# Kernel tuning notes

Hardware: AMD Instinct MI355X
Metric: run time of the kernel (lower is better)

The kernel has to match this reference:

```python
import jax, jax.numpy as jnp
import numpy as np

EPS = 1e-5

def _ln(x, g=None, b=None):
    m = x.mean(-1, keepdims=True)
    v = x.var(-1, keepdims=True)
    y = (x - m) / jnp.sqrt(v + EPS)
    if g is not None:
        y = y * g + b
    return y

def setup_inputs() -> dict:
    B, N, D, E, NC = 32, 256, 1024, 4096, 16
    key = jax.random.key(0)
    ks = iter(jax.random.split(key, 24))
    def rn(shape, s=0.02):
        return jax.random.normal(next(ks), shape, jnp.float32) * s
    return dict(
        h=jax.random.normal(next(ks), (B, N, D), jnp.float32),
        Wpp=rn((D, E)), bpp=jnp.zeros(E), Wsp=rn((D, E)), bsp=jnp.zeros(E),
        Wq=rn((E, E)), bq=jnp.zeros(E),
        Wk=rn((E, E)), bk=jnp.zeros(E),
        Wv=rn((E, E)), bv=jnp.zeros(E),
        g_pfs=jnp.ones(D + E), b_pfs=jnp.zeros(D + E),
        Wpfs=rn((D + E, D)), bpfs=jnp.zeros(D),
        g_sfs=jnp.ones(E), b_sfs=jnp.zeros(E),
        Wsfs=rn((E, D)), bsfs=jnp.zeros(D),
        Wpc=rn((D, NC)), bpc=jnp.zeros(NC),
        Wc0=rn((NC, 8, D)), bc0=jnp.zeros((NC, 8)),
        Wc1=rn((NC, 16, D)), bc1=jnp.zeros((NC, 16)),
        Wc2=rn((NC, 32, D)), bc2=jnp.zeros((NC, 32)),
    )

def reference(h, Wpp, bpp, Wsp, bsp, Wq, bq, Wk, bk, Wv, bv,
              g_pfs, b_pfs, Wpfs, bpfs, g_sfs, b_sfs, Wsfs, bsfs,
              Wpc, bpc, Wc0, bc0, Wc1, bc1, Wc2, bc2):
    B, N, D = h.shape
    H = 4
    E = Wpp.shape[1]
    hd = E // H
    scale = hd ** -0.5
    gelu = lambda x: jax.nn.gelu(x, approximate=False)  # torch exact GELU
    pp = gelu(h @ Wpp + bpp)                  # [B,N,E]
    sp = gelu(h @ Wsp + bsp)                  # [B,N,E]
    Q = (pp @ Wq + bq).reshape(B, N, H, hd)
    K = (sp @ Wk + bk).reshape(B, N, H, hd)
    V = (sp @ Wv + bv).reshape(B, N, H, hd)
    attn = jax.nn.softmax(jnp.einsum('bqhd,bkhd->bhqk', Q, K) * scale, axis=-1)
    intf = jnp.einsum('bhqk,bkhd->bqhd', attn, V).reshape(B, N, E)
    intf = _ln(intf)                          # F.layer_norm, no affine
    pvec = _ln((_ln(jnp.concatenate([h, intf], -1), g_pfs, b_pfs) @ Wpfs + bpfs).mean(1))  # [B,D]
    svec = _ln((_ln(sp, g_sfs, b_sfs) @ Wsfs + bsfs).mean(1))                               # [B,D]
    parent_logits = pvec @ Wpc + bpc          # [B,NC]
    y_hat = jnp.argmax(parent_logits, axis=1) # argmax(softmax) == argmax(logits)
    # routed child heads: gather per-sample weight by parent argmax, batched matvec
    child = tuple(
        jnp.einsum('bd,bnd->bn', svec, W[y_hat]) + b[y_hat]
        for W, b in ((Wc0, bc0), (Wc1, bc1), (Wc2, bc2))
    )
    return (parent_logits,) + child + (pvec, svec)
```

## Files before the change

kernel.cpp:

```cpp
#include <hip/hip_runtime.h>
#include <hip/hip_bf16.h>

typedef __bf16 bf16x8 __attribute__((ext_vector_type(8)));
typedef float f32x4 __attribute__((ext_vector_type(4)));
typedef unsigned long long u64;

#define EPSV 1e-5f

__device__ __forceinline__ float bf2f(unsigned short u){
  unsigned int x = ((unsigned int)u) << 16;
  return __builtin_bit_cast(float, x);
}
__device__ __forceinline__ unsigned short f2bf(float f){
  __bf16 b = (__bf16)f;
  return __builtin_bit_cast(unsigned short, b);
}
__device__ __forceinline__ float gelu_exact(float x){
  return 0.5f * x * (1.0f + erff(x * 0.7071067811865476f));
}
__device__ __forceinline__ void gload_lds16(const void* g, void* l){
  __builtin_amdgcn_global_load_lds((const __attribute__((address_space(1))) unsigned int*)g,
                                   (__attribute__((address_space(3))) unsigned int*)l, 16, 0, 0);
}

#define LGKM0() do{ asm volatile("s_waitcnt lgkmcnt(0)" ::: "memory"); __builtin_amdgcn_sched_barrier(0); }while(0)

template<int MODE>
__global__ __launch_bounds__(512, 2)
void gemm256(const unsigned short* __restrict__ A, const unsigned short* __restrict__ B,
             const float* __restrict__ bias, void* __restrict__ Cv,
             int Kd, int lda, int ldb, int ldc)
{
  __shared__ char smem[131072];
  const int t = threadIdx.x;
  const int w = t >> 6, l = t & 63;
  const int wm = w >> 2, wn = w & 3;
  const int lr = l & 15, lg = l >> 4;
  const int nbx = gridDim.x;
  const int nwg = nbx * gridDim.y;
  int bid = blockIdx.y*nbx + blockIdx.x;
  if ((nwg & 7) == 0) bid = (bid & 7)*(nwg >> 3) + (bid >> 3);
  const int bm0 = (bid / nbx) * 256, bn0 = (bid % nbx) * 256;
  const int nk = Kd >> 6;

  const int srow = t >> 3;
  const int sslot = t & 7;

  f32x4 acc[8][4];
  #pragma unroll
  for (int i=0;i<8;++i){
    #pragma unroll
    for (int j=0;j<4;++j){ f32x4 zz = {0.f,0.f,0.f,0.f}; acc[i][j] = zz; }
  }
  bf16x8 a0[4][2], a1[4][2], b0[2][2], b1[2][2];

  auto stage = [&](int kt, int mat, int hf, int q){
    if (kt >= nk) return;
    const int r_h = q*64 + srow;
    const int s_ = sslot ^ ((r_h >> 1) & 7);
    const unsigned short* gp = (mat ? B + (size_t)(bn0 + hf*128 + r_h)*ldb
                                    : A + (size_t)(bm0 + hf*128 + r_h)*lda)
                               + (kt << 6) + s_*8;
    char* lp = smem + mat*65536 + (kt&1)*32768 + hf*16384 + q*8192 + t*16;
    gload_lds16((const void*)gp, (void*)lp);
  };
  auto rdA = [&](int d, int fm, int kk)->bf16x8{
    const int r = fm*16 + lr;
    const int s_ = (kk*4 + lg) ^ ((r >> 1) & 7);
    return *(const bf16x8*)(smem + d*32768 + wm*16384 + r*128 + s_*16);
  };
  auto rdB = [&](int d, int fn, int kk)->bf16x8{
    const int r = (wn&1)*64 + fn*16 + lr;
    const int s_ = (kk*4 + lg) ^ ((r >> 1) & 7);
    return *(const bf16x8*)(smem + 65536 + d*32768 + (wn>>1)*16384 + r*128 + s_*16);
  };

  auto ktile = [&](int kt, int d){
    #pragma unroll
    for (int fm=0; fm<4; ++fm){ a0[fm][0] = rdA(d, fm, 0); a0[fm][1] = rdA(d, fm, 1); }
    #pragma unroll
    for (int fn=0; fn<2; ++fn){ b0[fn][0] = rdB(d, fn, 0); b0[fn][1] = rdB(d, fn, 1); }
    stage(kt+1, 0, 0, 1); stage(kt+1, 0, 1, 1);
    __builtin_amdgcn_s_barrier();
    LGKM0();
    __builtin_amdgcn_s_setprio(1);
    #pragma unroll
    for (int fm=0; fm<4; ++fm)
      #pragma unroll
      for (int fn=0; fn<2; ++fn)
        #pragma unroll
        for (int kk=0; kk<2; ++kk)
          acc[fm][fn] = __builtin_amdgcn_mfma_f32_16x16x32_bf16(a0[fm][kk], b0[fn][kk], acc[fm][fn], 0,0,0);
    __builtin_amdgcn_s_setprio(0);
    __builtin_amdgcn_s_barrier();
    #pragma unroll
    for (int fn=0; fn<2; ++fn){ b1[fn][0] = rdB(d, fn+2, 0); b1[fn][1] = rdB(d, fn+2, 1); }
    stage(kt+2, 0, 0, 0); stage(kt+2, 0, 1, 0);
    __builtin_amdgcn_s_barrier();
    LGKM0();
    __builtin_amdgcn_s_setprio(1);
    #pragma unroll
    for (int fm=0; fm<4; ++fm)
      #pragma unroll
      for (int fn=0; fn<2; ++fn)
        #pragma unroll
        for (int kk=0; kk<2; ++kk)
          acc[fm][fn+2] = __builtin_amdgcn_mfma_f32_16x16x32_bf16(a0[fm][kk], b1[fn][kk], acc[fm][fn+2], 0,0,0);
    __builtin_amdgcn_s_setprio(0);
    __builtin_amdgcn_s_barrier();
    #pragma unroll
    for (int fm=0; fm<4; ++fm){ a1[fm][0] = rdA(d, fm+4, 0); a1[fm][1] = rdA(d, fm+4, 1); }
    stage(kt+2, 1, 0, 0); stage(kt+2, 1, 1, 0);
    __builtin_amdgcn_s_barrier();
    LGKM0();
    __builtin_amdgcn_s_setprio(1);
    #pragma unroll
    for (int fm=0; fm<4; ++fm)
      #pragma unroll
      for (int fn=0; fn<2; ++fn)
        #pragma unroll
        for (int kk=0; kk<2; ++kk)
          acc[fm+4][fn+2] = __builtin_amdgcn_mfma_f32_16x16x32_bf16(a1[fm][kk], b1[fn][kk], acc[fm+4][fn+2], 0,0,0);
    __builtin_amdgcn_s_setprio(0);
    __builtin_amdgcn_s_barrier();
    stage(kt+2, 1, 0, 1); stage(kt+2, 1, 1, 1);
    __builtin_amdgcn_s_setprio(1);
    #pragma unroll
    for (int fm=0; fm<4; ++fm)
      #pragma unroll
      for (int fn=0; fn<2; ++fn)
        #pragma unroll
        for (int kk=0; kk<2; ++kk)
          acc[fm+4][fn] = __builtin_amdgcn_mfma_f32_16x16x32_bf16(a1[fm][kk], b0[fn][kk], acc[fm+4][fn], 0,0,0);
    __builtin_amdgcn_s_setprio(0);
    if (kt + 2 < nk) { asm volatile("s_waitcnt vmcnt(6)" ::: "memory"); }
    else             { asm volatile("s_waitcnt vmcnt(0)" ::: "memory"); }
    __builtin_amdgcn_s_barrier();
  };

  stage(0,0,0,0); stage(0,0,1,0); stage(0,0,0,1); stage(0,0,1,1);
  stage(0,1,0,0); stage(0,1,1,0); stage(0,1,0,1); stage(0,1,1,1);
  stage(1,0,0,0); stage(1,0,1,0);
  stage(1,1,0,0); stage(1,1,1,0); stage(1,1,0,1); stage(1,1,1,1);
  asm volatile("s_waitcnt vmcnt(6)" ::: "memory");
  __builtin_amdgcn_s_barrier();

  for (int kt = 0; kt < nk; kt += 2){ ktile(kt, 0); ktile(kt+1, 1); }

  #pragma unroll
  for (int fm=0; fm<8; ++fm){
    #pragma unroll
    for (int fn=0; fn<4; ++fn){
      const int row0 = bm0 + wm*128 + fm*16 + lg*4;
      const int col  = bn0 + wn*64 + fn*16 + lr;
      f32x4 v = acc[fm][fn];
      if constexpr (MODE == 3){
        unsigned short* C = (unsigned short*)Cv;
        const float bb = bias[col];
        u64 pack = 0;
        #pragma unroll
        for (int j=0;j<4;++j) pack |= (u64)f2bf(v[j] + bb) << (16*j);
        *(u64*)(C + (size_t)col*256 + (size_t)(row0>>8)*1048576 + (row0&255)) = pack;
      } else {
        unsigned short* C = (unsigned short*)Cv;
        const float bb = bias[col];
        #pragma unroll
        for (int j=0;j<4;++j){
          float x = v[j] + bb;
          if constexpr (MODE==0) x = gelu_exact(x);
          C[(size_t)(row0+j)*ldc + col] = f2bf(x);
        }
      }
    }
  }
}

template<int MODE>
__global__ __launch_bounds__(256)
void gemm_bt(const unsigned short* __restrict__ A, const unsigned short* __restrict__ B,
             const float* __restrict__ bias, void* __restrict__ Cv,
             int Kd, int lda, int ldb, int ldc,
             long sA2, long sA1, long sB2, long sB1, long sC2, long sC1,
             float scale)
{
  __shared__ unsigned short lds[2][2][4096];
  const int t = threadIdx.x;
  const int w = t >> 6, l = t & 63;
  const int z = blockIdx.z;
  A += (size_t)(z>>2)*sA2 + (size_t)(z&3)*sA1;
  B += (size_t)(z>>2)*sB2 + (size_t)(z&3)*sB1;
  const int bm0 = blockIdx.y * 128, bn0 = blockIdx.x * 128;
  const int nk = Kd >> 5;

  const int sr = l >> 2;
  const int ss = l & 3;

  f32x4 acc[4][4];
  #pragma unroll
  for (int i=0;i<4;++i){
    #pragma unroll
    for (int j=0;j<4;++j){ f32x4 zz = {0.f,0.f,0.f,0.f}; acc[i][j] = zz; }
  }

  const int wm = w >> 1, wn = w & 1;
  const int lr = l & 15, lg = l >> 4;

  auto stage = [&](int kt, int bb){
    const int k0 = kt << 5;
    #pragma unroll
    for (int i=0;i<2;++i){
      const int r  = w*32 + i*16 + sr;
      const int sa = ss ^ ((r>>1)&3);
      const unsigned short* ga = A + (size_t)(bm0 + r)*lda + (k0 + sa*8);
      gload_lds16((const void*)ga, (void*)((char*)&lds[bb][0][0] + w*2048 + i*1024));
      const unsigned short* gb = B + (size_t)(bn0 + r)*ldb + (k0 + sa*8);
      gload_lds16((const void*)gb, (void*)((char*)&lds[bb][1][0] + w*2048 + i*1024));
    }
  };

  int buf = 0;
  stage(0, 0);
  for (int kt=0; kt<nk; ++kt){
    __syncthreads();
    if (kt+1 < nk) stage(kt+1, buf^1);
    bf16x8 av[4], bv[4];
    #pragma unroll
    for (int fm=0; fm<4; ++fm){
      const int row = wm*64 + fm*16 + lr;
      const int sl  = lg ^ ((row>>1)&3);
      av[fm] = *(const bf16x8*)((const char*)&lds[buf][0][0] + row*64 + sl*16);
    }
    #pragma unroll
    for (int fn=0; fn<4; ++fn){
      const int col = wn*64 + fn*16 + lr;
      const int sl  = lg ^ ((col>>1)&3);
      bv[fn] = *(const bf16x8*)((const char*)&lds[buf][1][0] + col*64 + sl*16);
    }
    #pragma unroll
    for (int fm=0; fm<4; ++fm){
      #pragma unroll
      for (int fn=0; fn<4; ++fn)
        acc[fm][fn] = __builtin_amdgcn_mfma_f32_16x16x32_bf16(av[fm], bv[fn], acc[fm][fn], 0,0,0);
    }
    buf ^= 1;
  }

  const size_t coff = (size_t)(z>>2)*sC2 + (size_t)(z&3)*sC1;
  #pragma unroll
  for (int fm=0; fm<4; ++fm){
    #pragma unroll
    for (int fn=0; fn<4; ++fn){
      const int row0 = bm0 + wm*64 + fm*16 + lg*4;
      const int col  = bn0 + wn*64 + fn*16 + lr;
      f32x4 v = acc[fm][fn];
      if constexpr (MODE == 2){
        float* C = (float*)Cv + coff;
        #pragma unroll
        for (int j=0;j<4;++j) C[(size_t)(row0+j)*ldc + col] = v[j]*scale;
      }
    }
  }
}

__global__ __launch_bounds__(256)
void k_convh(const float* __restrict__ in, unsigned short* __restrict__ out){
  const size_t id = (size_t)blockIdx.x*256 + threadIdx.x;
  float4 v = ((const float4*)in)[id];
  u64 pack = (u64)f2bf(v.x) | ((u64)f2bf(v.y)<<16) | ((u64)f2bf(v.z)<<32) | ((u64)f2bf(v.w)<<48);
  *(u64*)(out + id*4) = pack;
}

__global__ __launch_bounds__(256)
void k_tconv(const float* __restrict__ W, unsigned short* __restrict__ Wt, int Kd, int N){
  __shared__ float lt[64][65];
  const int t = threadIdx.x;
  const int n0 = blockIdx.x*64, k0 = blockIdx.y*64;
  #pragma unroll
  for (int i=0;i<16;++i){
    int lin = i*256 + t; int r = lin>>6, c = lin&63;
    lt[r][c] = W[(size_t)(k0+r)*N + n0 + c];
  }
  __syncthreads();
  #pragma unroll
  for (int i=0;i<16;++i){
    int lin = i*256 + t; int n = lin>>6, k = lin&63;
    Wt[(size_t)(n0+n)*Kd + k0 + k] = f2bf(lt[k][n]);
  }
}

__global__ __launch_bounds__(256)
void k_softmax(const float* __restrict__ S, unsigned short* __restrict__ P){
  const int t = threadIdx.x, w = t>>6, l = t&63;
  const size_t row = (size_t)blockIdx.x*4 + w;
  float4 v = *(const float4*)(S + row*256 + l*4);
  float m = fmaxf(fmaxf(v.x,v.y), fmaxf(v.z,v.w));
  #pragma unroll
  for (int off=32; off; off>>=1) m = fmaxf(m, __shfl_xor(m, off));
  float e0 = expf(v.x-m), e1 = expf(v.y-m), e2 = expf(v.z-m), e3 = expf(v.w-m);
  float s = e0+e1+e2+e3;
  #pragma unroll
  for (int off=32; off; off>>=1) s += __shfl_xor(s, off);
  const float inv = 1.0f/s;
  u64 pack = (u64)f2bf(e0*inv) | ((u64)f2bf(e1*inv)<<16) | ((u64)f2bf(e2*inv)<<32) | ((u64)f2bf(e3*inv)<<48);
  *(u64*)(P + row*256 + l*4) = pack;
}

__device__ __forceinline__ void blkred2(float& a, float& b, float* sred, int t){
  #pragma unroll
  for (int off=32; off; off>>=1){ a += __shfl_xor(a, off); b += __shfl_xor(b, off); }
  __syncthreads();
  if ((t&63)==0){ sred[(t>>6)*2] = a; sred[(t>>6)*2+1] = b; }
  __syncthreads();
  a = sred[0]+sred[2]+sred[4]+sred[6];
  b = sred[1]+sred[3]+sred[5]+sred[7];
}

__global__ __launch_bounds__(256)
void k_stats(const float* __restrict__ h, const float* __restrict__ intf,
             const unsigned short* __restrict__ sp,
             const float* __restrict__ g_pfs, const float* __restrict__ b_pfs,
             const float* __restrict__ g_sfs, const float* __restrict__ b_sfs,
             float* __restrict__ part_p, float* __restrict__ part_s, int g0)
{
  __shared__ float sred[8];
  const int bl = blockIdx.x, grp = blockIdx.y, t = threadIdx.x;
  float zacc[20], wacc[16];
  #pragma unroll
  for (int j=0;j<20;++j) zacc[j]=0.f;
  #pragma unroll
  for (int j=0;j<16;++j) wacc[j]=0.f;
  for (int rr=0; rr<32; ++rr){
    const size_t r = (size_t)bl*256 + grp*32 + rr;
    float hv[4], iv[16], sv[16];
    #pragma unroll
    for (int j=0;j<4;++j) hv[j] = h[r*1024 + j*256 + t];
    float s1=0.f, s2=0.f;
    #pragma unroll
    for (int j=0;j<16;++j){ float x = intf[r*4096 + j*256 + t]; iv[j]=x; s1+=x; s2+=x*x; }
    blkred2(s1,s2,sred,t);
    const float m1 = s1*(1.f/4096.f);
    const float rs1 = rsqrtf(fmaxf(s2*(1.f/4096.f) - m1*m1, 0.f) + EPSV);
    float t1=0.f, t2=0.f;
    #pragma unroll
    for (int j=0;j<4;++j){ t1 += hv[j]; t2 += hv[j]*hv[j]; }
    #pragma unroll
    for (int j=0;j<16;++j){ float y = (iv[j]-m1)*rs1; iv[j]=y; t1+=y; t2+=y*y; }
    blkred2(t1,t2,sred,t);
    const float m2 = t1*(1.f/5120.f);
    const float rs2 = rsqrtf(fmaxf(t2*(1.f/5120.f) - m2*m2, 0.f) + EPSV);
    #pragma unroll
    for (int j=0;j<4;++j){ int idx = j*256+t; zacc[j] += ((hv[j]-m2)*rs2)*g_pfs[idx] + b_pfs[idx]; }
    #pragma unroll
    for (int j=0;j<16;++j){ int idx = 1024 + j*256+t; zacc[4+j] += ((iv[j]-m2)*rs2)*g_pfs[idx] + b_pfs[idx]; }
    float u1=0.f, u2=0.f;
    #pragma unroll
    for (int j=0;j<16;++j){ float x = bf2f(sp[r*4096 + j*256 + t]); sv[j]=x; u1+=x; u2+=x*x; }
    blkred2(u1,u2,sred,t);
    const float m3 = u1*(1.f/4096.f);
    const float rs3 = rsqrtf(fmaxf(u2*(1.f/4096.f) - m3*m3, 0.f) + EPSV);
    #pragma unroll
    for (int j=0;j<16;++j){ int idx = j*256+t; wacc[j] += ((sv[j]-m3)*rs3)*g_sfs[idx] + b_sfs[idx]; }
  }
  const size_t pb = (size_t)(g0 + bl)*8 + grp;
  #pragma unroll
  for (int j=0;j<20;++j) part_p[pb*5120 + j*256 + t] = zacc[j];
  #pragma unroll
  for (int j=0;j<16;++j) part_s[pb*4096 + j*256 + t] = wacc[j];
}

__global__ __launch_bounds__(256)
void k_reduce(const float* __restrict__ part_p, const float* __restrict__ part_s,
              float* __restrict__ xbar, float* __restrict__ ybar){
  int id = blockIdx.x*256 + threadIdx.x;
  if (id < 32*5120){
    const int b = id / 5120, i = id % 5120;
    float s = 0.f;
    for (int g=0; g<8; ++g) s += part_p[((size_t)b*8+g)*5120 + i];
    xbar[(size_t)b*5120 + i] = s * (1.f/256.f);
  } else {
    id -= 32*5120;
    const int b = id / 4096, i = id % 4096;
    float s = 0.f;
    for (int g=0; g<8; ++g) s += part_s[((size_t)b*8+g)*4096 + i];
    ybar[(size_t)b*4096 + i] = s * (1.f/256.f);
  }
}

__global__ __launch_bounds__(256)
void k_proj_part(const float* __restrict__ xbar, const float* __restrict__ ybar,
                 const float* __restrict__ Wpfs, const float* __restrict__ Wsfs,
                 float* __restrict__ pbuf){
  const int path = blockIdx.z;
  const int y = blockIdx.y;
  if (path == 1 && y >= 8) return;
  const int Kp = path ? 4096 : 5120;
  const float* X = path ? ybar : xbar;
  const float* W = path ? Wsfs : Wpfs;
  const int t = threadIdx.x;
  const int col = blockIdx.x*64 + (t & 63);
  const int sub = t >> 6;
  const int k0 = y*512 + sub*128;
  float acc[32];
  #pragma unroll
  for (int b=0;b<32;++b) acc[b] = 0.f;
  for (int i4=0; i4<32; ++i4){
    const int k = k0 + i4*4;
    float wv0 = W[(size_t)(k  )*1024 + col];
    float wv1 = W[(size_t)(k+1)*1024 + col];
    float wv2 = W[(size_t)(k+2)*1024 + col];
    float wv3 = W[(size_t)(k+3)*1024 + col];
    #pragma unroll
    for (int b=0;b<32;++b){
      float4 xv = *(const float4*)(X + (size_t)b*Kp + k);
      acc[b] += xv.x*wv0 + xv.y*wv1 + xv.z*wv2 + xv.w*wv3;
    }
  }
  float* dst = pbuf + ((size_t)(path*40 + y*4 + sub)*32)*1024 + col;
  #pragma unroll
  for (int b=0;b<32;++b) dst[(size_t)b*1024] = acc[b];
}

__global__ __launch_bounds__(256)
void k_projred(const float* __restrict__ pbuf,
               const float* __restrict__ bpfs, const float* __restrict__ bsfs,
               float* __restrict__ tpre, float* __restrict__ spre){
  const int id = blockIdx.x*256 + threadIdx.x;
  const int path = id >> 15;
  const int rem = id & 32767;
  const int b = rem >> 10, col = rem & 1023;
  const int ns = path ? 32 : 40;
  const float* src = pbuf + ((size_t)(path*40)*32 + b)*1024 + col;
  float s = path ? bsfs[col] : bpfs[col];
  for (int g=0; g<ns; ++g) s += src[(size_t)g*32*1024];
  (path ? spre : tpre)[(size_t)b*1024 + col] = s;
}

__global__ __launch_bounds__(256)
void k_lnrow(const float* __restrict__ tpre, const float* __restrict__ spre,
             float* __restrict__ out){
  __shared__ float sred[8];
  const int id = blockIdx.x, t = threadIdx.x;
  const int path = id >> 5, b = id & 31;
  const float* src = (path ? spre : tpre) + (size_t)b*1024;
  float v[4]; float s1=0.f, s2=0.f;
  #pragma unroll
  for (int j=0;j<4;++j){ v[j] = src[j*256+t]; s1 += v[j]; s2 += v[j]*v[j]; }
  blkred2(s1,s2,sred,t);
  const float m = s1*(1.f/1024.f);
  const float rs = rsqrtf(fmaxf(s2*(1.f/1024.f)-m*m,0.f)+EPSV);
  float* dst = out + (path ? 35072 : 2304) + (size_t)b*1024;
  #pragma unroll
  for (int j=0;j<4;++j) dst[j*256+t] = (v[j]-m)*rs;
}

__global__ __launch_bounds__(256)
void k_head(const float* __restrict__ Wpc, const float* __restrict__ bpc,
            const float* __restrict__ Wc0, const float* __restrict__ bc0,
            const float* __restrict__ Wc1, const float* __restrict__ bc1,
            const float* __restrict__ Wc2, const float* __restrict__ bc2,
            float* __restrict__ out){
  __shared__ float slog[16];
  __shared__ int sy;
  const int b = blockIdx.x, t = threadIdx.x, w = t>>6, l = t&63;
  const float* pv = out + 2304 + (size_t)b*1024;
  const float* sv = out + 35072 + (size_t)b*1024;
  #pragma unroll
  for (int jj=0; jj<4; ++jj){
    const int j = w*4 + jj;
    float a = 0.f;
    for (int i=l; i<1024; i+=64) a += pv[i]*Wpc[(size_t)i*16 + j];
    #pragma unroll
    for (int off=32; off; off>>=1) a += __shfl_xor(a, off);
    if (l==0){ const float lgv = a + bpc[j]; slog[j] = lgv; out[b*16 + j] = lgv; }
  }
  __syncthreads();
  if (t==0){
    int best=0; float bvv = slog[0];
    for (int i=1;i<16;++i) if (slog[i] > bvv){ bvv = slog[i]; best = i; }
    sy = best;
  }
  __syncthreads();
  const int y = sy;
  const float* Ws[3] = {Wc0, Wc1, Wc2};
  const float* bs[3] = {bc0, bc1, bc2};
  const int nouts[3] = {8,16,32};
  const int ooff[3]  = {512, 768, 1280};
  for (int hI=0; hI<3; ++hI){
    const int no = nouts[hI];
    for (int n = w; n < no; n += 4){
      const float* wr = Ws[hI] + ((size_t)y*no + n)*1024;
      float a = 0.f;
      for (int i=l; i<1024; i+=64) a += sv[i]*wr[i];
      #pragma unroll
      for (int off=32; off; off>>=1) a += __shfl_xor(a, off);
      if (l==0) out[ooff[hI] + b*no + n] = a + bs[hI][(size_t)y*no + n];
    }
  }
}

extern "C" void kernel_launch(void* const* d_in, const int* in_sizes, int n_in,
                              void* d_out, int out_size, void* d_ws, size_t ws_size,
                              hipStream_t stream)
{
  const float* h    = (const float*)d_in[0];
  const float* Wpp  = (const float*)d_in[1];
  const float* bpp  = (const float*)d_in[2];
  const float* Wsp  = (const float*)d_in[3];
  const float* bsp  = (const float*)d_in[4];
  const float* Wq   = (const float*)d_in[5];
  const float* bq   = (const float*)d_in[6];
  const float* Wk   = (const float*)d_in[7];
  const float* bk   = (const float*)d_in[8];
  const float* Wv   = (const float*)d_in[9];
  const float* bv   = (const float*)d_in[10];
  const float* g_pfs= (const float*)d_in[11];
  const float* b_pfs= (const float*)d_in[12];
  const float* Wpfs = (const float*)d_in[13];
  const float* bpfs = (const float*)d_in[14];
  const float* g_sfs= (const float*)d_in[15];
  const float* b_sfs= (const float*)d_in[16];
  const float* Wsfs = (const float*)d_in[17];
  const float* bsfs = (const float*)d_in[18];
  const float* Wpc  = (const float*)d_in[19];
  const float* bpc  = (const float*)d_in[20];
  const float* Wc0  = (const float*)d_in[21];
  const float* bc0  = (const float*)d_in[22];
  const float* Wc1  = (const float*)d_in[23];
  const float* bc1  = (const float*)d_in[24];
  const float* Wc2  = (const float*)d_in[25];
  const float* bc2  = (const float*)d_in[26];
  float* out = (float*)d_out;
  char* ws = (char*)d_ws;
  (void)in_sizes; (void)n_in; (void)out_size;

  struct PlanT { int G, NS, hoist; };
  const PlanT plans[10] = {
    {32,4096,0},{16,4096,1},{16,4096,0},{8,4096,1},{8,4096,0},
    {4,4096,0},{2,4096,0},{1,4096,0},{1,2048,0},{1,1024,0}};
  int G = 0, NS = 0, HOIST = 0;
  size_t oWt=0,oWpp=0,oWsp=0,oWq=0,oWk=0,oWv=0;
  size_t oPp=0,oPs=0,oXb=0,oYb=0,oTp=0,oSp=0,oPbf=0,oHb=0,oPb=0,oSb=0,oQ=0,oK=0,oVt=0,oS=0,oP=0;
  for (int pi = 0; pi < 10; ++pi){
    const size_t g = plans[pi].G, ns = plans[pi].NS;
    const int hoist = plans[pi].hoist;
    size_t off = 0;
    auto alloc = [&](size_t bytes){ size_t o = off; off += (bytes + 255) & ~255ULL; return o; };
    size_t wt=0, w1=0, w2=0, w3=0, w4=0, w5=0;
    if (hoist){
      w1 = alloc(1024ULL*4096*2); w2 = alloc(1024ULL*4096*2);
      w3 = alloc(4096ULL*4096*2); w4 = alloc(4096ULL*4096*2); w5 = alloc(4096ULL*4096*2);
    } else {
      wt = alloc(ns*4096*2);
    }
    size_t pp_ = alloc(32*8*5120*4);
    size_t ps_ = alloc(32*8*4096*4);
    size_t xb = alloc(32*5120*4);
    size_t yb = alloc(32*4096*4);
    size_t tp = alloc(32*1024*4);
    size_t sp_ = alloc(32*1024*4);
    size_t pbf = alloc(2*40*32*1024*4);
    size_t hb = alloc(g*524288);
    size_t pb = alloc(g*2097152);
    size_t sb = alloc(g*2097152);
    size_t q  = alloc(g*2097152);
    size_t k  = alloc(g*2097152);
    size_t vt = alloc(g*2097152);
    size_t s  = alloc(g*1048576);
    size_t p  = alloc(g*524288);
    if (off <= ws_size){
      G = (int)g; NS = (int)ns; HOIST = hoist;
      oWt=wt; oWpp=w1; oWsp=w2; oWq=w3; oWk=w4; oWv=w5;
      oPp=pp_; oPs=ps_; oXb=xb; oYb=yb; oTp=tp; oSp=sp_; oPbf=pbf;
      oHb=hb; oPb=pb; oSb=sb; oQ=q; oK=k; oVt=vt; oS=s; oP=p;
      break;
    }
  }
  if (!G) return;

  unsigned short* Wt   = (unsigned short*)(ws + oWt);
  unsigned short* WppT = (unsigned short*)(ws + oWpp);
  unsigned short* WspT = (unsigned short*)(ws + oWsp);
  unsigned short* WqT  = (unsigned short*)(ws + oWq);
  unsigned short* WkT  = (unsigned short*)(ws + oWk);
  unsigned short* WvT  = (unsigned short*)(ws + oWv);
  float* part_p = (float*)(ws + oPp);
  float* part_s = (float*)(ws + oPs);
  float* xbar   = (float*)(ws + oXb);
  float* ybar   = (float*)(ws + oYb);
  float* tpre   = (float*)(ws + oTp);
  float* spre   = (float*)(ws + oSp);
  float* pbuf   = (float*)(ws + oPbf);
  unsigned short* h_bf = (unsigned short*)(ws + oHb);
  unsigned short* pp   = (unsigned short*)(ws + oPb);
  unsigned short* sp   = (unsigned short*)(ws + oSb);
  unsigned short* Q    = (unsigned short*)(ws + oQ);
  unsigned short* Kb   = (unsigned short*)(ws + oK);
  unsigned short* Vt   = (unsigned short*)(ws + oVt);
  float*          S    = (float*)(ws + oS);
  unsigned short* P    = (unsigned short*)(ws + oP);
  float*          intf = (float*)(ws + oQ);

  const float scale = 1.0f/32.0f;
  (void)oK;

  if (HOIST){
    hipLaunchKernelGGL(k_tconv, dim3(64,16), dim3(256), 0, stream, Wpp, WppT, 1024, 4096);
    hipLaunchKernelGGL(k_tconv, dim3(64,16), dim3(256), 0, stream, Wsp, WspT, 1024, 4096);
    hipLaunchKernelGGL(k_tconv, dim3(64,64), dim3(256), 0, stream, Wq, WqT, 4096, 4096);
    hipLaunchKernelGGL(k_tconv, dim3(64,64), dim3(256), 0, stream, Wk, WkT, 4096, 4096);
    hipLaunchKernelGGL(k_tconv, dim3(64,64), dim3(256), 0, stream, Wv, WvT, 4096, 4096);
  }

  for (int g0 = 0; g0 < 32; g0 += G){
    const float* h_g = h + (size_t)g0*262144;

    hipLaunchKernelGGL(k_convh, dim3(G*256), dim3(256), 0, stream, h_g, h_bf);

    if (!HOIST) hipLaunchKernelGGL(k_tconv, dim3(64,16), dim3(256), 0, stream, Wpp, Wt, 1024, 4096);
    hipLaunchKernelGGL(gemm256<0>, dim3(16,G), dim3(512), 0, stream,
                       h_bf, HOIST?WppT:Wt, bpp, (void*)pp, 1024, 1024,1024,4096);
    if (HOIST){
      hipLaunchKernelGGL(gemm256<1>, dim3(16,G), dim3(512), 0, stream,
                         pp, WqT, bq, (void*)Q, 4096, 4096,4096,4096);
    } else {
      for (int nso = 0; nso < 4096; nso += NS){
        hipLaunchKernelGGL(k_tconv, dim3(NS/64,64), dim3(256), 0, stream, Wq + nso, Wt, 4096, 4096);
        hipLaunchKernelGGL(gemm256<1>, dim3(NS/256,G), dim3(512), 0, stream,
                           pp, Wt, bq + nso, (void*)(Q + nso), 4096, 4096,4096,4096);
      }
    }
    if (!HOIST) hipLaunchKernelGGL(k_tconv, dim3(64,16), dim3(256), 0, stream, Wsp, Wt, 1024, 4096);
    hipLaunchKernelGGL(gemm256<0>, dim3(16,G), dim3(512), 0, stream,
                       h_bf, HOIST?WspT:Wt, bsp, (void*)sp, 1024, 1024,1024,4096);
    if (HOIST){
      hipLaunchKernelGGL(gemm256<1>, dim3(16,G), dim3(512), 0, stream,
                         sp, WkT, bk, (void*)Kb, 4096, 4096,4096,4096);
    } else {
      for (int nso = 0; nso < 4096; nso += NS){
        hipLaunchKernelGGL(k_tconv, dim3(NS/64,64), dim3(256), 0, stream, Wk + nso, Wt, 4096, 4096);
        hipLaunchKernelGGL(gemm256<1>, dim3(NS/256,G), dim3(512), 0, stream,
                           sp, Wt, bk + nso, (void*)(Kb + nso), 4096, 4096,4096,4096);
      }
    }
    if (HOIST){
      hipLaunchKernelGGL(gemm256<3>, dim3(16,G), dim3(512), 0, stream,
                         sp, WvT, bv, (void*)Vt, 4096, 4096,4096,256);
    } else {
      for (int nso = 0; nso < 4096; nso += NS){
        hipLaunchKernelGGL(k_tconv, dim3(NS/64,64), dim3(256), 0, stream, Wv + nso, Wt, 4096, 4096);
        hipLaunchKernelGGL(gemm256<3>, dim3(NS/256,G), dim3(512), 0, stream,
                           sp, Wt, bv + nso, (void*)(Vt + (size_t)nso*256), 4096, 4096,4096,256);
      }
    }
    hipLaunchKernelGGL(gemm_bt<2>, dim3(2,2,G*4), dim3(256), 0, stream,
                       Q, Kb, (const float*)nullptr, (void*)S, 1024, 4096,4096,256,
                       1048576L,1024L, 1048576L,1024L, 262144L,65536L, scale);
    hipLaunchKernelGGL(k_softmax, dim3(G*256), dim3(256), 0, stream, S, P);
    hipLaunchKernelGGL(gemm_bt<2>, dim3(8,2,G*4), dim3(256), 0, stream,
                       P, Vt, (const float*)nullptr, (void*)intf, 256, 256,256,4096,
                       262144L,65536L, 1048576L,262144L, 1048576L,1024L, 1.f);
    hipLaunchKernelGGL(k_stats, dim3(G,8), dim3(256), 0, stream,
                       h_g, intf, sp, g_pfs, b_pfs, g_sfs, b_sfs, part_p, part_s, g0);
  }

  hipLaunchKernelGGL(k_reduce, dim3(1152), dim3(256), 0, stream, part_p, part_s, xbar, ybar);
  hipLaunchKernelGGL(k_proj_part, dim3(16,10,2), dim3(256), 0, stream,
                     xbar, ybar, Wpfs, Wsfs, pbuf);
  hipLaunchKernelGGL(k_projred, dim3(256), dim3(256), 0, stream,
                     pbuf, bpfs, bsfs, tpre, spre);
  hipLaunchKernelGGL(k_lnrow, dim3(64), dim3(256), 0, stream, tpre, spre, out);
  hipLaunchKernelGGL(k_head, dim3(32), dim3(256), 0, stream,
                     Wpc, bpc, Wc0, bc0, Wc1, bc1, Wc2, bc2, out);
}
```

Baseline: 1.511 ms.

## Fuse pp/sp and K/V projections into wide GEMMs and drop LDS waitcnt

Concatenates the transposed Wpp/Wsp weights and the Wk/Wv weights so that each pair of projections runs as one double-width GEMM launch. A new epilogue mode routes the upper column half to the second output, using the transposed V layout. It also adds a hoisted plan at G=32 and replaces the explicit lgkmcnt(0) wait before the MFMA blocks with only a sched_barrier. That relies on the compiler inserting the needed LDS waits, which risks correctness or a worse schedule. Fewer launches and larger grids should improve GPU fill and cut launch overhead.

```diff
diff --git a/kernel.cpp b/kernel.cpp
--- a/kernel.cpp
+++ b/kernel.cpp
@@ -23,12 +23,11 @@
                                    (__attribute__((address_space(3))) unsigned int*)l, 16, 0, 0);
 }
 
-#define LGKM0() do{ asm volatile("s_waitcnt lgkmcnt(0)" ::: "memory"); __builtin_amdgcn_sched_barrier(0); }while(0)
-
 template<int MODE>
 __global__ __launch_bounds__(512, 2)
 void gemm256(const unsigned short* __restrict__ A, const unsigned short* __restrict__ B,
-             const float* __restrict__ bias, void* __restrict__ Cv,
+             const float* __restrict__ bias0, const float* __restrict__ bias1,
+             void* __restrict__ C0v, void* __restrict__ C1v,
              int Kd, int lda, int ldb, int ldc)
 {
   __shared__ char smem[131072];
@@ -82,7 +81,7 @@
     for (int fn=0; fn<2; ++fn){ b0[fn][0] = rdB(d, fn, 0); b0[fn][1] = rdB(d, fn, 1); }
     stage(kt+1, 0, 0, 1); stage(kt+1, 0, 1, 1);
     __builtin_amdgcn_s_barrier();
-    LGKM0();
+    __builtin_amdgcn_sched_barrier(0);
     __builtin_amdgcn_s_setprio(1);
     #pragma unroll
     for (int fm=0; fm<4; ++fm)
@@ -97,7 +96,7 @@
     for (int fn=0; fn<2; ++fn){ b1[fn][0] = rdB(d, fn+2, 0); b1[fn][1] = rdB(d, fn+2, 1); }
     stage(kt+2, 0, 0, 0); stage(kt+2, 0, 1, 0);
     __builtin_amdgcn_s_barrier();
-    LGKM0();
+    __builtin_amdgcn_sched_barrier(0);
     __builtin_amdgcn_s_setprio(1);
     #pragma unroll
     for (int fm=0; fm<4; ++fm)
@@ -112,7 +111,7 @@
     for (int fm=0; fm<4; ++fm){ a1[fm][0] = rdA(d, fm+4, 0); a1[fm][1] = rdA(d, fm+4, 1); }
     stage(kt+2, 1, 0, 0); stage(kt+2, 1, 1, 0);
     __builtin_amdgcn_s_barrier();
-    LGKM0();
+    __builtin_amdgcn_sched_barrier(0);
     __builtin_amdgcn_s_setprio(1);
     #pragma unroll
     for (int fm=0; fm<4; ++fm)
@@ -155,20 +154,37 @@
       const int col  = bn0 + wn*64 + fn*16 + lr;
       f32x4 v = acc[fm][fn];
       if constexpr (MODE == 3){
-        unsigned short* C = (unsigned short*)Cv;
-        const float bb = bias[col];
+        unsigned short* C = (unsigned short*)C0v;
+        const float bb = bias0[col];
         u64 pack = 0;
         #pragma unroll
         for (int j=0;j<4;++j) pack |= (u64)f2bf(v[j] + bb) << (16*j);
         *(u64*)(C + (size_t)col*256 + (size_t)(row0>>8)*1048576 + (row0&255)) = pack;
+      } else if constexpr (MODE == 4){
+        if (col < 4096){
+          unsigned short* C = (unsigned short*)C0v;
+          const float bb = bias0[col];
+          #pragma unroll
+          for (int j=0;j<4;++j) C[(size_t)(row0+j)*ldc + col] = f2bf(v[j] + bb);
+        } else {
+          const int c2 = col - 4096;
+          unsigned short* C = (unsigned short*)C1v;
+          const float bb = bias1[c2];
+          u64 pack = 0;
+          #pragma unroll
+          for (int j=0;j<4;++j) pack |= (u64)f2bf(v[j] + bb) << (16*j);
+          *(u64*)(C + (size_t)c2*256 + (size_t)(row0>>8)*1048576 + (row0&255)) = pack;
+        }
       } else {
-        unsigned short* C = (unsigned short*)Cv;
-        const float bb = bias[col];
+        const bool hi = (MODE == 0) && (col >= 4096);
+        unsigned short* C = (unsigned short*)(hi ? C1v : C0v);
+        const int c2 = hi ? (col - 4096) : col;
+        const float bb = hi ? bias1[c2] : bias0[c2];
         #pragma unroll
         for (int j=0;j<4;++j){
           float x = v[j] + bb;
           if constexpr (MODE==0) x = gelu_exact(x);
-          C[(size_t)(row0+j)*ldc + col] = f2bf(x);
+          C[(size_t)(row0+j)*ldc + c2] = f2bf(x);
         }
       }
     }
@@ -534,21 +550,22 @@
   (void)in_sizes; (void)n_in; (void)out_size;
 
   struct PlanT { int G, NS, hoist; };
-  const PlanT plans[10] = {
-    {32,4096,0},{16,4096,1},{16,4096,0},{8,4096,1},{8,4096,0},
+  const PlanT plans[11] = {
+    {32,4096,1},{32,4096,0},{16,4096,1},{16,4096,0},{8,4096,1},{8,4096,0},
     {4,4096,0},{2,4096,0},{1,4096,0},{1,2048,0},{1,1024,0}};
   int G = 0, NS = 0, HOIST = 0;
-  size_t oWt=0,oWpp=0,oWsp=0,oWq=0,oWk=0,oWv=0;
+  size_t oWt=0,oWps=0,oWq=0,oWkv=0;
   size_t oPp=0,oPs=0,oXb=0,oYb=0,oTp=0,oSp=0,oPbf=0,oHb=0,oPb=0,oSb=0,oQ=0,oK=0,oVt=0,oS=0,oP=0;
-  for (int pi = 0; pi < 10; ++pi){
+  for (int pi = 0; pi < 11; ++pi){
     const size_t g = plans[pi].G, ns = plans[pi].NS;
     const int hoist = plans[pi].hoist;
     size_t off = 0;
     auto alloc = [&](size_t bytes){ size_t o = off; off += (bytes + 255) & ~255ULL; return o; };
-    size_t wt=0, w1=0, w2=0, w3=0, w4=0, w5=0;
+    size_t wt=0, wps=0, wq=0, wkv=0;
     if (hoist){
-      w1 = alloc(1024ULL*4096*2); w2 = alloc(1024ULL*4096*2);
-      w3 = alloc(4096ULL*4096*2); w4 = alloc(4096ULL*4096*2); w5 = alloc(4096ULL*4096*2);
+      wps = alloc(8192ULL*1024*2);
+      wq  = alloc(4096ULL*4096*2);
+      wkv = alloc(8192ULL*4096*2);
     } else {
       wt = alloc(ns*4096*2);
     }
@@ -569,7 +586,7 @@
     size_t p  = alloc(g*524288);
     if (off <= ws_size){
       G = (int)g; NS = (int)ns; HOIST = hoist;
-      oWt=wt; oWpp=w1; oWsp=w2; oWq=w3; oWk=w4; oWv=w5;
+      oWt=wt; oWps=wps; oWq=wq; oWkv=wkv;
       oPp=pp_; oPs=ps_; oXb=xb; oYb=yb; oTp=tp; oSp=sp_; oPbf=pbf;
       oHb=hb; oPb=pb; oSb=sb; oQ=q; oK=k; oVt=vt; oS=s; oP=p;
       break;
@@ -578,11 +595,9 @@
   if (!G) return;
 
   unsigned short* Wt   = (unsigned short*)(ws + oWt);
-  unsigned short* WppT = (unsigned short*)(ws + oWpp);
-  unsigned short* WspT = (unsigned short*)(ws + oWsp);
+  unsigned short* WpsT = (unsigned short*)(ws + oWps);
   unsigned short* WqT  = (unsigned short*)(ws + oWq);
-  unsigned short* WkT  = (unsigned short*)(ws + oWk);
-  unsigned short* WvT  = (unsigned short*)(ws + oWv);
+  unsigned short* WkvT = (unsigned short*)(ws + oWkv);
   float* part_p = (float*)(ws + oPp);
   float* part_s = (float*)(ws + oPs);
   float* xbar   = (float*)(ws + oXb);
@@ -604,11 +619,11 @@
   (void)oK;
 
   if (HOIST){
-    hipLaunchKernelGGL(k_tconv, dim3(64,16), dim3(256), 0, stream, Wpp, WppT, 1024, 4096);
-    hipLaunchKernelGGL(k_tconv, dim3(64,16), dim3(256), 0, stream, Wsp, WspT, 1024, 4096);
+    hipLaunchKernelGGL(k_tconv, dim3(64,16), dim3(256), 0, stream, Wpp, WpsT, 1024, 4096);
+    hipLaunchKernelGGL(k_tconv, dim3(64,16), dim3(256), 0, stream, Wsp, WpsT + 4096ULL*1024, 1024, 4096);
     hipLaunchKernelGGL(k_tconv, dim3(64,64), dim3(256), 0, stream, Wq, WqT, 4096, 4096);
-    hipLaunchKernelGGL(k_tconv, dim3(64,64), dim3(256), 0, stream, Wk, WkT, 4096, 4096);
-    hipLaunchKernelGGL(k_tconv, dim3(64,64), dim3(256), 0, stream, Wv, WvT, 4096, 4096);
+    hipLaunchKernelGGL(k_tconv, dim3(64,64), dim3(256), 0, stream, Wk, WkvT, 4096, 4096);
+    hipLaunchKernelGGL(k_tconv, dim3(64,64), dim3(256), 0, stream, Wv, WkvT + 4096ULL*4096, 4096, 4096);
   }
 
   for (int g0 = 0; g0 < 32; g0 += G){
@@ -616,40 +631,34 @@
 
     hipLaunchKernelGGL(k_convh, dim3(G*256), dim3(256), 0, stream, h_g, h_bf);
 
-    if (!HOIST) hipLaunchKernelGGL(k_tconv, dim3(64,16), dim3(256), 0, stream, Wpp, Wt, 1024, 4096);
-    hipLaunchKernelGGL(gemm256<0>, dim3(16,G), dim3(512), 0, stream,
-                       h_bf, HOIST?WppT:Wt, bpp, (void*)pp, 1024, 1024,1024,4096);
     if (HOIST){
+      hipLaunchKernelGGL(gemm256<0>, dim3(32,G), dim3(512), 0, stream,
+                         h_bf, WpsT, bpp, bsp, (void*)pp, (void*)sp, 1024, 1024,1024,4096);
       hipLaunchKernelGGL(gemm256<1>, dim3(16,G), dim3(512), 0, stream,
-                         pp, WqT, bq, (void*)Q, 4096, 4096,4096,4096);
+                         pp, WqT, bq, bq, (void*)Q, (void*)Q, 4096, 4096,4096,4096);
+      hipLaunchKernelGGL(gemm256<4>, dim3(32,G), dim3(512), 0, stream,
+                         sp, WkvT, bk, bv, (void*)Kb, (void*)Vt, 4096, 4096,4096,4096);
     } else {
+      hipLaunchKernelGGL(k_tconv, dim3(64,16), dim3(256), 0, stream, Wpp, Wt, 1024, 4096);
+      hipLaunchKernelGGL(gemm256<0>, dim3(16,G), dim3(512), 0, stream,
+                         h_bf, Wt, bpp, bpp, (void*)pp, (void*)pp, 1024, 1024,1024,4096);
       for (int nso = 0; nso < 4096; nso += NS){
         hipLaunchKernelGGL(k_tconv, dim3(NS/64,64), dim3(256), 0, stream, Wq + nso, Wt, 4096, 4096);
         hipLaunchKernelGGL(gemm256<1>, dim3(NS/256,G), dim3(512), 0, stream,
-                           pp, Wt, bq + nso, (void*)(Q + nso), 4096, 4096,4096,4096);
+                           pp, Wt, bq + nso, bq + nso, (void*)(Q + nso), (void*)(Q + nso), 4096, 4096,4096,4096);
       }
-    }
-    if (!HOIST) hipLaunchKernelGGL(k_tconv, dim3(64,16), dim3(256), 0, stream, Wsp, Wt, 1024, 4096);
-    hipLaunchKernelGGL(gemm256<0>, dim3(16,G), dim3(512), 0, stream,
-                       h_bf, HOIST?WspT:Wt, bsp, (void*)sp, 1024, 1024,1024,4096);
-    if (HOIST){
-      hipLaunchKernelGGL(gemm256<1>, dim3(16,G), dim3(512), 0, stream,
-                         sp, WkT, bk, (void*)Kb, 4096, 4096,4096,4096);
-    } else {
+      hipLaunchKernelGGL(k_tconv, dim3(64,16), dim3(256), 0, stream, Wsp, Wt, 1024, 4096);
+      hipLaunchKernelGGL(gemm256<0>, dim3(16,G), dim3(512), 0, stream,
+                         h_bf, Wt, bsp, bsp, (void*)sp, (void*)sp, 1024, 1024,1024,4096);
       for (int nso = 0; nso < 4096; nso += NS){
         hipLaunchKernelGGL(k_tconv, dim3(NS/64,64), dim3(256), 0, stream, Wk + nso, Wt, 4096, 4096);
         hipLaunchKernelGGL(gemm256<1>, dim3(NS/256,G), dim3(512), 0, stream,
-                           sp, Wt, bk + nso, (void*)(Kb + nso), 4096, 4096,4096,4096);
+                           sp, Wt, bk + nso, bk + nso, (void*)(Kb + nso), (void*)(Kb + nso), 4096, 4096,4096,4096);
       }
-    }
-    if (HOIST){
-      hipLaunchKernelGGL(gemm256<3>, dim3(16,G), dim3(512), 0, stream,
-                         sp, WvT, bv, (void*)Vt, 4096, 4096,4096,256);
-    } else {
       for (int nso = 0; nso < 4096; nso += NS){
         hipLaunchKernelGGL(k_tconv, dim3(NS/64,64), dim3(256), 0, stream, Wv + nso, Wt, 4096, 4096);
         hipLaunchKernelGGL(gemm256<3>, dim3(NS/256,G), dim3(512), 0, stream,
-                           sp, Wt, bv + nso, (void*)(Vt + (size_t)nso*256), 4096, 4096,4096,256);
+                           sp, Wt, bv + nso, bv + nso, (void*)(Vt + (size_t)nso*256), (void*)(Vt + (size_t)nso*256), 4096, 4096,4096,256);
       }
     }
     hipLaunchKernelGGL(gemm_bt<2>, dim3(2,2,G*4), dim3(256), 0, stream,
```

Result: no change. 1.518 ms (+0.5%).
